# Kernel optimization log

Hardware: AMD Instinct MI355X
Metric: run time of the kernel (lower is better)

Reference implementation:

```python
import jax, jax.numpy as jnp
import numpy as np

N = 100_000          # nodes
E = 1_600_000        # edges (avg degree 16)
IN_DIM = 128
POS_DIM = 16
CONTENT_DIM = IN_DIM - POS_DIM   # 112
H = 4                # num_heads
D = 32               # out_dim per head (H*D == IN_DIM -> identity residual)
D4 = D // 4          # pos feature dim per head


def setup_inputs() -> dict:
    key = jax.random.key(0)
    ks = jax.random.split(key, 10)
    feat = jax.random.normal(ks[0], (N, IN_DIM), jnp.float32)
    src = jax.random.randint(ks[1], (E,), 0, N, jnp.int32)
    dst = jax.random.randint(ks[2], (E,), 0, N, jnp.int32)
    # learned parameters (xavier-ish scale)
    Wc = jax.random.normal(ks[3], (H * D, CONTENT_DIM), jnp.float32) * (1.0 / np.sqrt(CONTENT_DIM))
    Wp = jax.random.normal(ks[4], (H * D4, POS_DIM), jnp.float32) * (1.0 / np.sqrt(POS_DIM))
    attn_src = jax.random.normal(ks[5], (1, H, D), jnp.float32) * 0.1
    attn_dst = jax.random.normal(ks[6], (1, H, D), jnp.float32) * 0.1
    pos_attn_src = jax.random.normal(ks[7], (1, H, D4), jnp.float32) * 0.1
    pos_attn_dst = jax.random.normal(ks[8], (1, H, D4), jnp.float32) * 0.1
    att_comb = jnp.full((H, 2), 0.5, jnp.float32)  # nn.init.constant_(0.5)
    return {"feat": feat, "src": src, "dst": dst, "Wc": Wc, "Wp": Wp,
            "attn_src": attn_src, "attn_dst": attn_dst,
            "pos_attn_src": pos_attn_src, "pos_attn_dst": pos_attn_dst,
            "att_comb": att_comb}


def reference(feat, src, dst, Wc, Wp, attn_src, attn_dst,
              pos_attn_src, pos_attn_dst, att_comb):
    content = feat[:, :-POS_DIM]                       # [N, CONTENT_DIM]
    pos = feat[:, -POS_DIM:]                           # [N, POS_DIM]
    hc = (content @ Wc.T).reshape(N, H, D)             # [N, H, D]
    hp = (pos @ Wp.T).reshape(N, H, D4)                # [N, H, D4]

    # per-node attention projections (reduce over feature dim once)
    es = jnp.einsum('nhd,hd->nh', hc, attn_src[0])     # [N, H]
    ed = jnp.einsum('nhd,hd->nh', hc, attn_dst[0])
    ps = jnp.einsum('nhd,hd->nh', hp, pos_attn_src[0])
    pd = jnp.einsum('nhd,hd->nh', hp, pos_attn_dst[0])

    # per-edge combined score + leaky relu (slope 0.2)
    content_e = es[src] + ed[dst]                      # [E, H]
    pos_e = ps[src] + pd[dst]
    e = content_e * att_comb[:, 0] + pos_e * att_comb[:, 1]
    e = jnp.where(e > 0, e, 0.2 * e)

    # edge softmax grouped by destination node
    emax = jax.ops.segment_max(e, dst, num_segments=N)     # [N, H]
    ex = jnp.exp(e - emax[dst])
    esum = jax.ops.segment_sum(ex, dst, num_segments=N)    # [N, H]
    a = ex / esum[dst]                                     # [E, H]

    # weighted message aggregation: ft[v] = sum_{(u,v)} a_uv * hc[u]
    ft = jax.ops.segment_sum(a[:, :, None] * hc[src], dst, num_segments=N)  # [N, H, D]

    h = ft.reshape(N, H * D) + feat   # identity residual (in_dim == out_dim*num_heads)
    diversity_loss = jnp.zeros((), jnp.float32)  # eval path
    return h, diversity_loss
```

## Files before the change

### kernel.cpp

```cpp
#include <hip/hip_runtime.h>
#include <hip/hip_bf16.h>

#define NN 100000
#define NE 1600000
#define FD 128
#define CD 112
#define PDIM 16
#define NH 4
#define NB_SCAN 391
#define NSHARD 8
#define SHARD 12500
#define NE4 400000
#define NB_E4 1563

#define NOUT 144
#define MBLK 64
#define LDS_STRIDE 136
#define WT_U (MBLK * LDS_STRIDE)
#define NGB 1563
#define FUSE_GRID (NGB * 9)

using bf16x8 = __attribute__((ext_vector_type(8))) short;
using f32x4  = __attribute__((ext_vector_type(4))) float;

__device__ __forceinline__ unsigned short f2bf(float x) {
    union { float f; unsigned int u; } v; v.f = x;
    return (unsigned short)((v.u + 0x7fffu + ((v.u >> 16) & 1u)) >> 16);
}
__device__ __forceinline__ float bf_lo(unsigned int u) { return __uint_as_float(u << 16); }
__device__ __forceinline__ float bf_hi(unsigned int u) { return __uint_as_float(u & 0xffff0000u); }

__global__ __launch_bounds__(256) void prep_kernel(
    const float* __restrict__ Wc, const float* __restrict__ Wp,
    const float* __restrict__ attn_src, const float* __restrict__ attn_dst,
    const float* __restrict__ pos_attn_src, const float* __restrict__ pos_attn_dst,
    const float* __restrict__ att_comb, unsigned short* __restrict__ wt)
{
    __shared__ float sA[NH * FD], sB[NH * FD];
    const int t = threadIdx.x;
    #pragma unroll
    for (int r = 0; r < 2; ++r) {
        const int idx = t + r * 256;
        const int h = idx >> 7, k = idx & 127;
        const float c0 = att_comb[h * 2], c1 = att_comb[h * 2 + 1];
        float sa = 0.f, sb = 0.f;
        if (k < CD) {
            #pragma unroll 8
            for (int d = 0; d < 32; ++d) {
                const float wv = Wc[(size_t)(h * 32 + d) * CD + k];
                sa = fmaf(wv, attn_src[h * 32 + d], sa);
                sb = fmaf(wv, attn_dst[h * 32 + d], sb);
            }
            sa *= c0; sb *= c0;
        } else {
            const int k2 = k - CD;
            #pragma unroll
            for (int d4 = 0; d4 < 8; ++d4) {
                const float wv = Wp[(h * 8 + d4) * PDIM + k2];
                sa = fmaf(wv, pos_attn_src[h * 8 + d4], sa);
                sb = fmaf(wv, pos_attn_dst[h * 8 + d4], sb);
            }
            sa *= c1; sb *= c1;
        }
        sA[idx] = sa; sB[idx] = sb;
    }
    __syncthreads();
    #pragma unroll
    for (int it = 0; it < 72; ++it) {
        const int e = t + it * 256;
        const int row = e >> 7, k = e & 127;
        float val;
        if (row < 128)      val = (k < CD) ? Wc[(size_t)row * CD + k] : 0.f;
        else if (row < 132) val = sA[(row - 128) * FD + k];
        else if (row < 136) val = sB[(row - 132) * FD + k];
        else                val = 0.f;
        wt[e] = f2bf(val);
    }
}

__global__ __launch_bounds__(256) void mfma_hist_kernel(
    const float* __restrict__ feat, const unsigned short* __restrict__ wt,
    unsigned short* __restrict__ hc_bf, float* __restrict__ A,
    float* __restrict__ B, const int* __restrict__ dst, int* __restrict__ deg)
{
    __shared__ __align__(16) unsigned short sm[WT_U + NOUT * LDS_STRIDE];
    const int bid = blockIdx.x;
    const int g = bid / 9, r9 = bid % 9;
    const int t = threadIdx.x;

    if (r9 != 0) {
        const int histid = g * 8 + (r9 - 1);
        const int shard = histid & (NSHARD - 1);
        const int i4 = (histid >> 3) * 256 + t;
        if (i4 >= NE4) return;
        const int4 d4 = ((const int4*)dst)[i4];
        const int lo = shard * SHARD, hi = lo + SHARD;
        if (d4.x >= lo && d4.x < hi) atomicAdd(&deg[d4.x], 1);
        if (d4.y >= lo && d4.y < hi) atomicAdd(&deg[d4.y], 1);
        if (d4.z >= lo && d4.z < hi) atomicAdd(&deg[d4.z], 1);
        if (d4.w >= lo && d4.w < hi) atomicAdd(&deg[d4.w], 1);
        return;
    }

    unsigned int* smu = (unsigned int*)sm;
    const int n0 = g * MBLK;

    #pragma unroll
    for (int it = 0; it < 8; ++it) {
        const int e4 = t + it * 256;
        const int row = e4 >> 5, c4 = e4 & 31;
        uint2 packed = make_uint2(0u, 0u);
        if (n0 + row < NN) {
            const float4 gv = ((const float4*)(feat + (size_t)n0 * FD))[e4];
            packed.x = (unsigned int)f2bf(gv.x) | ((unsigned int)f2bf(gv.y) << 16);
            packed.y = (unsigned int)f2bf(gv.z) | ((unsigned int)f2bf(gv.w) << 16);
        }
        *(uint2*)&smu[row * (LDS_STRIDE / 2) + c4 * 2] = packed;
    }
    const uint4* wtu4 = (const uint4*)wt;
    #pragma unroll
    for (int it = 0; it < 9; ++it) {
        const int u4 = t + it * 256;
        const int row = u4 >> 4, c16 = u4 & 15;
        *(uint4*)&smu[WT_U / 2 + row * (LDS_STRIDE / 2) + c16 * 4] = wtu4[u4];
    }
    __syncthreads();

    const int w = t >> 6;
    const int lane = t & 63;
    const int mr = lane & 15, quad = lane >> 4;

    f32x4 acc[9];
    #pragma unroll
    for (int i = 0; i < 9; ++i) acc[i] = (f32x4){0.f, 0.f, 0.f, 0.f};

    #pragma unroll
    for (int kk = 0; kk < 4; ++kk) {
        const bf16x8 a =
            *(const bf16x8*)&sm[(w * 16 + mr) * LDS_STRIDE + kk * 32 + quad * 8];
        #pragma unroll
        for (int tt = 0; tt < 9; ++tt) {
            const bf16x8 b = *(const bf16x8*)&sm[WT_U + (tt * 16 + mr) * LDS_STRIDE +
                                                 kk * 32 + quad * 8];
            acc[tt] = __builtin_amdgcn_mfma_f32_16x16x32_bf16(a, b, acc[tt], 0, 0, 0);
        }
    }

    #pragma unroll
    for (int tt = 0; tt < 8; ++tt) {
        const int col = tt * 16 + mr;
        #pragma unroll
        for (int rr = 0; rr < 4; ++rr) {
            const int node = n0 + w * 16 + quad * 4 + rr;
            if (node < NN) hc_bf[(size_t)node * FD + col] = f2bf(acc[tt][rr]);
        }
    }
    #pragma unroll
    for (int rr = 0; rr < 4; ++rr) {
        const int node = n0 + w * 16 + quad * 4 + rr;
        if (node < NN) {
            if (mr < 4)      A[(size_t)node * NH + mr] = acc[8][rr];
            else if (mr < 8) B[(size_t)node * NH + (mr - 4)] = acc[8][rr];
        }
    }
}

__global__ __launch_bounds__(256) void scan1_kernel(const int* __restrict__ deg,
                                                    int* __restrict__ tmp,
                                                    int* __restrict__ bsum) {
    __shared__ int sh[256];
    const int t = threadIdx.x, b = blockIdx.x, i = b * 256 + t;
    const int v = (i < NN) ? deg[i] : 0;
    sh[t] = v;
    __syncthreads();
    #pragma unroll
    for (int off = 1; off < 256; off <<= 1) {
        const int x = (t >= off) ? sh[t - off] : 0;
        __syncthreads();
        sh[t] += x;
        __syncthreads();
    }
    if (i < NN) tmp[i] = sh[t] - v;
    if (t == 255) bsum[b] = sh[t];
}

__global__ __launch_bounds__(512) void scan2_kernel(int* __restrict__ bsum) {
    __shared__ int sh[512];
    const int t = threadIdx.x;
    const int v = (t < NB_SCAN) ? bsum[t] : 0;
    sh[t] = v;
    __syncthreads();
    #pragma unroll
    for (int off = 1; off < 512; off <<= 1) {
        const int x = (t >= off) ? sh[t - off] : 0;
        __syncthreads();
        sh[t] += x;
        __syncthreads();
    }
    if (t < NB_SCAN) bsum[t] = sh[t] - v;
}

__global__ __launch_bounds__(256) void scan3_kernel(const int* __restrict__ tmp,
                                                    const int* __restrict__ bsum,
                                                    int* __restrict__ row_ptr,
                                                    int* __restrict__ cursor) {
    const int i = blockIdx.x * 256 + threadIdx.x;
    if (i < NN) {
        const int v = tmp[i] + bsum[blockIdx.x];
        row_ptr[i] = v;
        cursor[i] = v;
    }
    if (i == 0) row_ptr[NN] = NE;
}

__global__ __launch_bounds__(256) void scatter_kernel(
    const int* __restrict__ src, const int* __restrict__ dst,
    int* __restrict__ cursor, int* __restrict__ col)
{
    const int shard = blockIdx.x & (NSHARD - 1);
    const int i4 = (blockIdx.x >> 3) * 256 + threadIdx.x;
    if (i4 >= NE4) return;
    const int4 d4 = ((const int4*)dst)[i4];
    const int4 s4 = ((const int4*)src)[i4];
    const int lo = shard * SHARD, hi = lo + SHARD;
    if (d4.x >= lo && d4.x < hi) col[atomicAdd(&cursor[d4.x], 1)] = s4.x;
    if (d4.y >= lo && d4.y < hi) col[atomicAdd(&cursor[d4.y], 1)] = s4.y;
    if (d4.z >= lo && d4.z < hi) col[atomicAdd(&cursor[d4.z], 1)] = s4.z;
    if (d4.w >= lo && d4.w < hi) col[atomicAdd(&cursor[d4.w], 1)] = s4.w;
}

__global__ __launch_bounds__(256) void agg_kernel(
    const int* __restrict__ row_ptr, const int* __restrict__ col,
    const float* __restrict__ A, const float* __restrict__ B,
    const uint2* __restrict__ hc_u2,
    const float* __restrict__ feat, float* __restrict__ out)
{
    const int n = blockIdx.x * 8 + (threadIdx.x >> 5);
    const int il = threadIdx.x & 31;
    const int hme = il >> 3;
    const int hbase = threadIdx.x & 0x20;
    const int gbase = hbase | (il & 0x18);
    const int r0 = row_ptr[n], r1 = row_ptr[n + 1];
    const float bh = B[(size_t)n * NH + hme];

    float ssum = 0.f;
    float acc0 = 0.f, acc1 = 0.f, acc2 = 0.f, acc3 = 0.f;

    int p = r0;
    while (p < r1) {
        const int cnt = (r1 - p < 32) ? (r1 - p) : 32;
        const int cidx = (il < cnt) ? col[p + il] : 0;
        for (int q = 0; q < cnt; q += 16) {
            const int j = il & 7;
            const int myc0 = __shfl(cidx, hbase | (q + j));
            const int myc1 = __shfl(cidx, hbase | (q + 8 + j));
            float w0 = 0.f, w1 = 0.f;
            if (q + j < cnt) {
                float e = A[(size_t)myc0 * NH + hme] + bh;
                e = e > 0.f ? e : 0.2f * e;
                w0 = __expf(e);
            }
            if (q + 8 + j < cnt) {
                float e = A[(size_t)myc1 * NH + hme] + bh;
                e = e > 0.f ? e : 0.2f * e;
                w1 = __expf(e);
            }
            int cm[16];
            #pragma unroll
            for (int m = 0; m < 16; ++m)
                cm[m] = __shfl(cidx, hbase | (q + m));
            uint2 u[16];
            #pragma unroll
            for (int m = 0; m < 16; ++m)
                u[m] = hc_u2[(size_t)cm[m] * 32 + il];
            #pragma unroll
            for (int m = 0; m < 16; ++m) {
                const float wm = (m < 8) ? __shfl(w0, gbase | m)
                                         : __shfl(w1, gbase | (m - 8));
                ssum += wm;
                acc0 = fmaf(wm, bf_lo(u[m].x), acc0);
                acc1 = fmaf(wm, bf_hi(u[m].x), acc1);
                acc2 = fmaf(wm, bf_lo(u[m].y), acc2);
                acc3 = fmaf(wm, bf_hi(u[m].y), acc3);
            }
        }
        p += cnt;
    }

    const float inv = ssum > 0.f ? 1.f / ssum : 0.f;
    const float4 fv = ((const float4*)(feat + (size_t)n * FD))[il];
    float4 ov;
    ov.x = acc0 * inv + fv.x;
    ov.y = acc1 * inv + fv.y;
    ov.z = acc2 * inv + fv.z;
    ov.w = acc3 * inv + fv.w;
    ((float4*)(out + (size_t)n * FD))[il] = ov;

    if (blockIdx.x == 0 && threadIdx.x == 0) out[(size_t)NN * FD] = 0.f;
}

extern "C" void kernel_launch(void* const* d_in, const int* in_sizes, int n_in,
                              void* d_out, int out_size, void* d_ws, size_t ws_size,
                              hipStream_t stream) {
    const float* feat         = (const float*)d_in[0];
    const int*   src          = (const int*)d_in[1];
    const int*   dst          = (const int*)d_in[2];
    const float* Wc           = (const float*)d_in[3];
    const float* Wp           = (const float*)d_in[4];
    const float* attn_src     = (const float*)d_in[5];
    const float* attn_dst     = (const float*)d_in[6];
    const float* pos_attn_src = (const float*)d_in[7];
    const float* pos_attn_dst = (const float*)d_in[8];
    const float* att_comb     = (const float*)d_in[9];
    float* out = (float*)d_out;

    char* w = (char*)d_ws;
    unsigned short* hc_bf = (unsigned short*)w;        w += (size_t)NN * FD * 2;
    float* A       = (float*)w;                        w += (size_t)NN * NH * 4;
    float* B       = (float*)w;                        w += (size_t)NN * NH * 4;
    int*   deg     = (int*)w;                          w += (size_t)NN * 4;
    int*   tmp     = (int*)w;                          w += (size_t)NN * 4;
    int*   row_ptr = (int*)w;                          w += (size_t)(NN + 4) * 4;
    int*   cursor  = (int*)w;                          w += (size_t)NN * 4;
    int*   bsum    = (int*)w;                          w += 512 * 4;
    unsigned short* wt = (unsigned short*)w;           w += (size_t)NOUT * FD * 2;
    int*   col     = (int*)w;

    hipMemsetAsync(deg, 0, (size_t)NN * sizeof(int), stream);
    prep_kernel<<<1, 256, 0, stream>>>(Wc, Wp, attn_src, attn_dst,
                                       pos_attn_src, pos_attn_dst, att_comb, wt);
    mfma_hist_kernel<<<FUSE_GRID, 256, 0, stream>>>(feat, wt, hc_bf, A, B, dst, deg);
    scan1_kernel<<<NB_SCAN, 256, 0, stream>>>(deg, tmp, bsum);
    scan2_kernel<<<1, 512, 0, stream>>>(bsum);
    scan3_kernel<<<NB_SCAN, 256, 0, stream>>>(tmp, bsum, row_ptr, cursor);
    scatter_kernel<<<NSHARD * NB_E4, 256, 0, stream>>>(src, dst, cursor, col);
    agg_kernel<<<NN / 8, 256, 0, stream>>>(row_ptr, col, A, B,
                                           (const uint2*)hc_bf, feat, out);
}
```

Before: 348.6 us.

## Regroup kernels: fuse histogram with prep, MFMA projection with scatter

```diff
diff --git a/kernel.cpp b/kernel.cpp
--- a/kernel.cpp
+++ b/kernel.cpp
@@ -12,11 +12,10 @@
 #define SHARD 12500
 #define NE4 400000
 #define NB_E4 1563
+#define NB_HIST (NSHARD * NB_E4)
 
 #define NOUT 144
 #define MBLK 64
-#define LDS_STRIDE 136
-#define WT_U (MBLK * LDS_STRIDE)
 #define NGB 1563
 #define FUSE_GRID (NGB * 9)
 
@@ -30,7 +29,17 @@
 __device__ __forceinline__ float bf_lo(unsigned int u) { return __uint_as_float(u << 16); }
 __device__ __forceinline__ float bf_hi(unsigned int u) { return __uint_as_float(u & 0xffff0000u); }
 
-__global__ __launch_bounds__(256) void prep_kernel(
+__device__ __forceinline__ bf16x8 pack8(const float4 g0, const float4 g1) {
+    bf16x8 r;
+    r[0] = (short)f2bf(g0.x); r[1] = (short)f2bf(g0.y);
+    r[2] = (short)f2bf(g0.z); r[3] = (short)f2bf(g0.w);
+    r[4] = (short)f2bf(g1.x); r[5] = (short)f2bf(g1.y);
+    r[6] = (short)f2bf(g1.z); r[7] = (short)f2bf(g1.w);
+    return r;
+}
+
+__global__ __launch_bounds__(256) void hist_prep_kernel(
+    const int* __restrict__ dst, int* __restrict__ deg,
     const float* __restrict__ Wc, const float* __restrict__ Wp,
     const float* __restrict__ attn_src, const float* __restrict__ attn_dst,
     const float* __restrict__ pos_attn_src, const float* __restrict__ pos_attn_dst,
@@ -38,6 +47,18 @@
 {
     __shared__ float sA[NH * FD], sB[NH * FD];
     const int t = threadIdx.x;
+    if (blockIdx.x < NB_HIST) {
+        const int shard = blockIdx.x & (NSHARD - 1);
+        const int i4 = (blockIdx.x >> 3) * 256 + t;
+        if (i4 >= NE4) return;
+        const int4 d4 = ((const int4*)dst)[i4];
+        const int lo = shard * SHARD, hi = lo + SHARD;
+        if (d4.x >= lo && d4.x < hi) atomicAdd(&deg[d4.x], 1);
+        if (d4.y >= lo && d4.y < hi) atomicAdd(&deg[d4.y], 1);
+        if (d4.z >= lo && d4.z < hi) atomicAdd(&deg[d4.z], 1);
+        if (d4.w >= lo && d4.w < hi) atomicAdd(&deg[d4.w], 1);
+        return;
+    }
     #pragma unroll
     for (int r = 0; r < 2; ++r) {
         const int idx = t + r * 256;
@@ -78,93 +99,6 @@
     }
 }
 
-__global__ __launch_bounds__(256) void mfma_hist_kernel(
-    const float* __restrict__ feat, const unsigned short* __restrict__ wt,
-    unsigned short* __restrict__ hc_bf, float* __restrict__ A,
-    float* __restrict__ B, const int* __restrict__ dst, int* __restrict__ deg)
-{
-    __shared__ __align__(16) unsigned short sm[WT_U + NOUT * LDS_STRIDE];
-    const int bid = blockIdx.x;
-    const int g = bid / 9, r9 = bid % 9;
-    const int t = threadIdx.x;
-
-    if (r9 != 0) {
-        const int histid = g * 8 + (r9 - 1);
-        const int shard = histid & (NSHARD - 1);
-        const int i4 = (histid >> 3) * 256 + t;
-        if (i4 >= NE4) return;
-        const int4 d4 = ((const int4*)dst)[i4];
-        const int lo = shard * SHARD, hi = lo + SHARD;
-        if (d4.x >= lo && d4.x < hi) atomicAdd(&deg[d4.x], 1);
-        if (d4.y >= lo && d4.y < hi) atomicAdd(&deg[d4.y], 1);
-        if (d4.z >= lo && d4.z < hi) atomicAdd(&deg[d4.z], 1);
-        if (d4.w >= lo && d4.w < hi) atomicAdd(&deg[d4.w], 1);
-        return;
-    }
-
-    unsigned int* smu = (unsigned int*)sm;
-    const int n0 = g * MBLK;
-
-    #pragma unroll
-    for (int it = 0; it < 8; ++it) {
-        const int e4 = t + it * 256;
-        const int row = e4 >> 5, c4 = e4 & 31;
-        uint2 packed = make_uint2(0u, 0u);
-        if (n0 + row < NN) {
-            const float4 gv = ((const float4*)(feat + (size_t)n0 * FD))[e4];
-            packed.x = (unsigned int)f2bf(gv.x) | ((unsigned int)f2bf(gv.y) << 16);
-            packed.y = (unsigned int)f2bf(gv.z) | ((unsigned int)f2bf(gv.w) << 16);
-        }
-        *(uint2*)&smu[row * (LDS_STRIDE / 2) + c4 * 2] = packed;
-    }
-    const uint4* wtu4 = (const uint4*)wt;
-    #pragma unroll
-    for (int it = 0; it < 9; ++it) {
-        const int u4 = t + it * 256;
-        const int row = u4 >> 4, c16 = u4 & 15;
-        *(uint4*)&smu[WT_U / 2 + row * (LDS_STRIDE / 2) + c16 * 4] = wtu4[u4];
-    }
-    __syncthreads();
-
-    const int w = t >> 6;
-    const int lane = t & 63;
-    const int mr = lane & 15, quad = lane >> 4;
-
-    f32x4 acc[9];
-    #pragma unroll
-    for (int i = 0; i < 9; ++i) acc[i] = (f32x4){0.f, 0.f, 0.f, 0.f};
-
-    #pragma unroll
-    for (int kk = 0; kk < 4; ++kk) {
-        const bf16x8 a =
-            *(const bf16x8*)&sm[(w * 16 + mr) * LDS_STRIDE + kk * 32 + quad * 8];
-        #pragma unroll
-        for (int tt = 0; tt < 9; ++tt) {
-            const bf16x8 b = *(const bf16x8*)&sm[WT_U + (tt * 16 + mr) * LDS_STRIDE +
-                                                 kk * 32 + quad * 8];
-            acc[tt] = __builtin_amdgcn_mfma_f32_16x16x32_bf16(a, b, acc[tt], 0, 0, 0);
-        }
-    }
-
-    #pragma unroll
-    for (int tt = 0; tt < 8; ++tt) {
-        const int col = tt * 16 + mr;
-        #pragma unroll
-        for (int rr = 0; rr < 4; ++rr) {
-            const int node = n0 + w * 16 + quad * 4 + rr;
-            if (node < NN) hc_bf[(size_t)node * FD + col] = f2bf(acc[tt][rr]);
-        }
-    }
-    #pragma unroll
-    for (int rr = 0; rr < 4; ++rr) {
-        const int node = n0 + w * 16 + quad * 4 + rr;
-        if (node < NN) {
-            if (mr < 4)      A[(size_t)node * NH + mr] = acc[8][rr];
-            else if (mr < 8) B[(size_t)node * NH + (mr - 4)] = acc[8][rr];
-        }
-    }
-}
-
 __global__ __launch_bounds__(256) void scan1_kernel(const int* __restrict__ deg,
                                                     int* __restrict__ tmp,
                                                     int* __restrict__ bsum) {
@@ -213,20 +147,72 @@
     if (i == 0) row_ptr[NN] = NE;
 }
 
-__global__ __launch_bounds__(256) void scatter_kernel(
+__global__ __launch_bounds__(256) void scatter_mfma_kernel(
     const int* __restrict__ src, const int* __restrict__ dst,
-    int* __restrict__ cursor, int* __restrict__ col)
+    int* __restrict__ cursor, int* __restrict__ col,
+    const float* __restrict__ feat, const unsigned short* __restrict__ wt,
+    unsigned short* __restrict__ hc_bf, float* __restrict__ A,
+    float* __restrict__ B)
 {
-    const int shard = blockIdx.x & (NSHARD - 1);
-    const int i4 = (blockIdx.x >> 3) * 256 + threadIdx.x;
-    if (i4 >= NE4) return;
-    const int4 d4 = ((const int4*)dst)[i4];
-    const int4 s4 = ((const int4*)src)[i4];
-    const int lo = shard * SHARD, hi = lo + SHARD;
-    if (d4.x >= lo && d4.x < hi) col[atomicAdd(&cursor[d4.x], 1)] = s4.x;
-    if (d4.y >= lo && d4.y < hi) col[atomicAdd(&cursor[d4.y], 1)] = s4.y;
-    if (d4.z >= lo && d4.z < hi) col[atomicAdd(&cursor[d4.z], 1)] = s4.z;
-    if (d4.w >= lo && d4.w < hi) col[atomicAdd(&cursor[d4.w], 1)] = s4.w;
+    const int bid = blockIdx.x;
+    const int g = bid / 9, r9 = bid % 9;
+    const int t = threadIdx.x;
+
+    if (r9 != 0) {
+        const int sid = g * 8 + (r9 - 1);
+        const int shard = sid & (NSHARD - 1);
+        const int i4 = (sid >> 3) * 256 + t;
+        if (i4 >= NE4) return;
+        const int4 d4 = ((const int4*)dst)[i4];
+        const int4 s4 = ((const int4*)src)[i4];
+        const int lo = shard * SHARD, hi = lo + SHARD;
+        if (d4.x >= lo && d4.x < hi) col[atomicAdd(&cursor[d4.x], 1)] = s4.x;
+        if (d4.y >= lo && d4.y < hi) col[atomicAdd(&cursor[d4.y], 1)] = s4.y;
+        if (d4.z >= lo && d4.z < hi) col[atomicAdd(&cursor[d4.z], 1)] = s4.z;
+        if (d4.w >= lo && d4.w < hi) col[atomicAdd(&cursor[d4.w], 1)] = s4.w;
+        return;
+    }
+
+    const int n0 = g * MBLK;
+    const int w = t >> 6;
+    const int lane = t & 63;
+    const int mr = lane & 15, quad = lane >> 4;
+    const int node_row = n0 + w * 16 + mr;
+    const size_t frow = (size_t)(node_row < NN ? node_row : 0) * FD;
+
+    f32x4 acc[9];
+    #pragma unroll
+    for (int i = 0; i < 9; ++i) acc[i] = (f32x4){0.f, 0.f, 0.f, 0.f};
+
+    #pragma unroll
+    for (int kk = 0; kk < 4; ++kk) {
+        const float4* fp = (const float4*)(feat + frow + kk * 32 + quad * 8);
+        const bf16x8 a = pack8(fp[0], fp[1]);
+        #pragma unroll
+        for (int tt = 0; tt < 9; ++tt) {
+            const bf16x8 b =
+                *(const bf16x8*)&wt[(size_t)(tt * 16 + mr) * FD + kk * 32 + quad * 8];
+            acc[tt] = __builtin_amdgcn_mfma_f32_16x16x32_bf16(a, b, acc[tt], 0, 0, 0);
+        }
+    }
+
+    #pragma unroll
+    for (int tt = 0; tt < 8; ++tt) {
+        const int colc = tt * 16 + mr;
+        #pragma unroll
+        for (int rr = 0; rr < 4; ++rr) {
+            const int node = n0 + w * 16 + quad * 4 + rr;
+            if (node < NN) hc_bf[(size_t)node * FD + colc] = f2bf(acc[tt][rr]);
+        }
+    }
+    #pragma unroll
+    for (int rr = 0; rr < 4; ++rr) {
+        const int node = n0 + w * 16 + quad * 4 + rr;
+        if (node < NN) {
+            if (mr < 4)      A[(size_t)node * NH + mr] = acc[8][rr];
+            else if (mr < 8) B[(size_t)node * NH + (mr - 4)] = acc[8][rr];
+        }
+    }
 }
 
 __global__ __launch_bounds__(256) void agg_kernel(
@@ -251,6 +237,14 @@
         const int cnt = (r1 - p < 32) ? (r1 - p) : 32;
         const int cidx = (il < cnt) ? col[p + il] : 0;
         for (int q = 0; q < cnt; q += 16) {
+            int cm[16];
+            #pragma unroll
+            for (int m = 0; m < 16; ++m)
+                cm[m] = __shfl(cidx, hbase | (q + m));
+            uint2 u[16];
+            #pragma unroll
+            for (int m = 0; m < 16; ++m)
+                u[m] = hc_u2[(size_t)cm[m] * 32 + il];
             const int j = il & 7;
             const int myc0 = __shfl(cidx, hbase | (q + j));
             const int myc1 = __shfl(cidx, hbase | (q + 8 + j));
@@ -265,14 +259,7 @@
                 e = e > 0.f ? e : 0.2f * e;
                 w1 = __expf(e);
             }
-            int cm[16];
-            #pragma unroll
-            for (int m = 0; m < 16; ++m)
-                cm[m] = __shfl(cidx, hbase | (q + m));
-            uint2 u[16];
-            #pragma unroll
-            for (int m = 0; m < 16; ++m)
-                u[m] = hc_u2[(size_t)cm[m] * 32 + il];
+            __builtin_amdgcn_sched_barrier(0);
             #pragma unroll
             for (int m = 0; m < 16; ++m) {
                 const float wm = (m < 8) ? __shfl(w0, gbase | m)
@@ -327,13 +314,13 @@
     int*   col     = (int*)w;
 
     hipMemsetAsync(deg, 0, (size_t)NN * sizeof(int), stream);
-    prep_kernel<<<1, 256, 0, stream>>>(Wc, Wp, attn_src, attn_dst,
-                                       pos_attn_src, pos_attn_dst, att_comb, wt);
-    mfma_hist_kernel<<<FUSE_GRID, 256, 0, stream>>>(feat, wt, hc_bf, A, B, dst, deg);
+    hist_prep_kernel<<<NB_HIST + 1, 256, 0, stream>>>(dst, deg, Wc, Wp,
+        attn_src, attn_dst, pos_attn_src, pos_attn_dst, att_comb, wt);
     scan1_kernel<<<NB_SCAN, 256, 0, stream>>>(deg, tmp, bsum);
     scan2_kernel<<<1, 512, 0, stream>>>(bsum);
     scan3_kernel<<<NB_SCAN, 256, 0, stream>>>(tmp, bsum, row_ptr, cursor);
-    scatter_kernel<<<NSHARD * NB_E4, 256, 0, stream>>>(src, dst, cursor, col);
+    scatter_mfma_kernel<<<FUSE_GRID, 256, 0, stream>>>(src, dst, cursor, col,
+        feat, wt, hc_bf, A, B);
     agg_kernel<<<NN / 8, 256, 0, stream>>>(row_ptr, col, A, B,
                                            (const uint2*)hc_bf, feat, out);
 }
```

New measurement: 384.0 us. 10.2% more time.
